# Performance work log

Hardware: AMD Instinct MI355X
Metric: run time of the kernel (lower is better)

Reference implementation:

```python
import jax, jax.numpy as jnp
import numpy as np

FACTOR = 1
EPS = 1e-8
SCALES = (1, 2, 4)


def _pool(x, scale):
    # adaptive_avg_pool1d along time with L % scale == 0 -> uniform bin mean
    if scale == 1:
        return x
    B, L, H, E = x.shape
    return x.reshape(B, L // scale, scale, H, E).mean(axis=2)


def _interp_linear(x, L_out):
    # F.interpolate(mode='linear', align_corners=False) along time axis (axis=1)
    B, Ls, H, E = x.shape
    i = jnp.arange(L_out, dtype=jnp.float32)
    src = jnp.maximum((i + 0.5) * (Ls / L_out) - 0.5, 0.0)
    x0 = jnp.floor(src).astype(jnp.int32)
    x1 = jnp.minimum(x0 + 1, Ls - 1)
    lam = (src - x0.astype(jnp.float32))[None, :, None, None]
    return x[:, x0] * (1.0 - lam) + x[:, x1] * lam


def _corr_agg(q, k, v, w1, b1, w2, b2, w3, b3):
    # q,k,v: [B, Ls, H, E]
    B, Ls, H, E = q.shape
    qf = jnp.fft.rfft(q.transpose(0, 2, 3, 1), axis=-1)   # [B,H,E,Lf]
    kf = jnp.fft.rfft(k.transpose(0, 2, 3, 1), axis=-1)
    corr = jnp.fft.irfft(qf * jnp.conj(kf), n=Ls, axis=-1).astype(jnp.float32)  # [B,H,E,Ls]

    # ---- adaptive-k features ----
    energy = jnp.mean(jnp.sum(corr ** 2, axis=(1, 2)))          # scalar, expanded to B
    var = jnp.var(corr.reshape(B, -1), axis=1, ddof=1)          # unbiased, like torch.var
    cm = corr.reshape(B, H * E, Ls).mean(axis=1)                # [B, Ls]
    pk = jnp.sum((cm[:, 1:-1] > cm[:, :-2]) & (cm[:, 1:-1] > cm[:, 2:]), axis=1).astype(jnp.float32)
    feats = jnp.stack([jnp.broadcast_to(energy, (B,)), var, pk], axis=1)  # [B,3]
    h = jax.nn.relu(feats @ w1.T + b1)
    h = jax.nn.relu(h @ w2.T + b2)
    ratio = jax.nn.sigmoid(h @ w3.T + b3)[:, 0]                 # [B]
    kvals = jnp.clip((ratio * Ls * FACTOR).astype(jnp.int32), 1, Ls)  # [B]

    # ---- adaptive time-delay aggregation ----
    c = corr.transpose(0, 3, 1, 2)                              # [B, Ls, H, E]
    interior = (c[:, 1:-1] > c[:, :-2]) & (c[:, 1:-1] > c[:, 2:])
    pad = jnp.zeros((B, 1, H, E), dtype=bool)
    peaks = jnp.concatenate([pad, interior, pad], axis=1)       # [B,Ls,H,E] local maxima

    neg_inf = jnp.float32(-jnp.inf)
    vals = jnp.where(peaks, c, neg_inf).reshape(B, -1)
    count = peaks.reshape(B, -1).sum(axis=1)
    sorted_desc = -jnp.sort(-vals, axis=1)
    thresh = jnp.take_along_axis(sorted_desc, (kvals - 1)[:, None], axis=1)[:, 0]  # k-th largest peak
    topk_mask = peaks & (c >= thresh[:, None, None, None])
    keep_topk = (count > kvals)[:, None, None, None]
    final = jnp.where(keep_topk, topk_mask, peaks)

    attn = jnp.where(final, c, 0.0)
    w = jax.nn.softmax(attn + EPS, axis=1)                      # softmax over time lags
    return w * v                                                # einsum('lhe,lhe->lhe') == elementwise


def setup_inputs() -> dict:
    key = jax.random.key(0)
    ks = jax.random.split(key, 10)
    B, L, H, E = 16, 1024, 8, 64
    return {
        "queries": jax.random.normal(ks[0], (B, L, H, E), jnp.float32),
        "keys": jax.random.normal(ks[1], (B, L, H, E), jnp.float32),
        "values": jax.random.normal(ks[2], (B, L, H, E), jnp.float32),
        "scale_weights": jax.random.normal(ks[3], (3,), jnp.float32) * 0.1 + 1.0 / 3.0,
        "k_w1": jax.random.normal(ks[4], (32, 3), jnp.float32) * 0.1,
        "k_b1": jax.random.normal(ks[5], (32,), jnp.float32) * 0.1,
        "k_w2": jax.random.normal(ks[6], (16, 32), jnp.float32) * 0.1,
        "k_b2": jax.random.normal(ks[7], (16,), jnp.float32) * 0.1,
        "k_w3": jax.random.normal(ks[8], (1, 16), jnp.float32) * 0.1,
        "k_b3": jax.random.normal(ks[9], (1,), jnp.float32) * 0.1,
    }


def reference(queries, keys, values, scale_weights, k_w1, k_b1, k_w2, k_b2, k_w3, k_b3):
    B, L, H, E = queries.shape
    out = jnp.zeros_like(queries)
    for i, scale in enumerate(SCALES):
        q, k, v = _pool(queries, scale), _pool(keys, scale), _pool(values, scale)
        o = _corr_agg(q, k, v, k_w1, k_b1, k_w2, k_b2, k_w3, k_b3)
        if scale > 1:
            o = _interp_linear(o, L)
        out = out + o * scale_weights[i]
    return out
```

## Files before the change

kernel.cpp:

```cpp
#include <hip/hip_runtime.h>
#include <math.h>

typedef unsigned int u32;
typedef unsigned long long u64;

#define B_ 16
#define L_ 1024
#define H_ 8
#define E_ 64
#define C_ 512
#define NB_SEL 8
#define GCH 8
#define TC 32
#define CAPR 160

__device__ __forceinline__ size_t co(int sidx) {
  return sidx == 0 ? 0u : (sidx == 1 ? 8388608u : 12582912u);
}
__device__ __forceinline__ u32 pk_off(int sidx) {
  return sidx == 0 ? 0u : (sidx == 1 ? 3211264u : 4816896u);
}
__device__ __forceinline__ u32 pk_cap(int sidx) { return 200704u >> sidx; }

__device__ __forceinline__ u32 f2key(float f) {
  u32 u = __float_as_uint(f);
  return (u & 0x80000000u) ? ~u : (u | 0x80000000u);
}
__device__ __forceinline__ float key2f(u32 k) {
  u32 u = (k & 0x80000000u) ? (k ^ 0x80000000u) : ~k;
  return __uint_as_float(u);
}

__global__ void k_init(u32* histA, u32* histB, u32* peak_cnt, u32* done,
                       double* s1, double* s2, float* cm) {
  const int gid = blockIdx.x * 256 + threadIdx.x;
  const int gs = gridDim.x * 256;
  for (int i = gid; i < 3 * 16 * 256; i += gs) { histA[i] = 0; histB[i] = 0; }
  for (int i = gid; i < 3 * 16 * 1024; i += gs) cm[i] = 0.f;
  for (int i = gid; i < 3 * 16 * 16; i += gs) peak_cnt[i] = 0;
  for (int i = gid; i < 144; i += gs) done[i] = 0;
  for (int i = gid; i < 48; i += gs) { s1[i] = 0.0; s2[i] = 0.0; }
}

template<int S>
__device__ __forceinline__ float4 pool_load(const float* gp) {
  float4 v = *(const float4*)gp;
  if constexpr (S >= 2) {
    float4 v2 = *(const float4*)(gp + C_);
    v.x += v2.x; v.y += v2.y; v.z += v2.z; v.w += v2.w;
  }
  if constexpr (S == 4) {
    float4 v3 = *(const float4*)(gp + 2 * C_);
    float4 v4 = *(const float4*)(gp + 3 * C_);
    v.x += v3.x + v4.x; v.y += v3.y + v4.y;
    v.z += v3.z + v4.z; v.w += v3.w + v4.w;
  }
  constexpr float sc = (S == 1) ? 1.f : (S == 2) ? 0.5f : 0.25f;
  if constexpr (S >= 2) { v.x *= sc; v.y *= sc; v.z *= sc; v.w *= sc; }
  return v;
}

template<int S>
__launch_bounds__(256, 3)
__global__ void k_corr(const float* __restrict__ Q, const float* __restrict__ K,
                       float* __restrict__ corr) {
  constexpr int LS = 1024 / S;
  constexpr int LMASK = LS - 1;
  constexpr int NCHUNK = LS / TC;
  __shared__ float qs[TC * 64];
  __shared__ float ks[CAPR * 64];
  const int tid = threadIdx.x;
  const int e = tid & 63;
  const int slot32 = __builtin_amdgcn_readfirstlane((tid >> 6) << 5);
  const int bh = blockIdx.x;
  const int tau0 = blockIdx.y << 7;
  const int b = bh >> 3, h = bh & 7;
  const size_t gbase = (size_t)b * L_ * C_ + (size_t)h * 64;
  const int l16 = tid & 15;
  const int rbase = tid >> 4;
  const int bp0 = 96 - slot32;

  float acc[32];
#pragma unroll
  for (int i = 0; i < 32; ++i) acc[i] = 0.f;

  float4 pq0, pq1, pk0, pk1;
  if constexpr (S == 1) {
    pq0 = *(const float4*)(Q + gbase + (size_t)rbase * C_ + l16 * 4);
    pq1 = *(const float4*)(Q + gbase + (size_t)(rbase + 16) * C_ + l16 * 4);
  }

  int cph = 0;
  for (int chunk = 0; chunk < NCHUNK; ++chunk) {
    const int t0 = chunk * TC;
    __syncthreads();
    if constexpr (S == 1) {
      *(float4*)(qs + rbase * 64 + l16 * 4) = pq0;
      *(float4*)(qs + (rbase + 16) * 64 + l16 * 4) = pq1;
      if (chunk == 0) {
#pragma unroll
        for (int it = 0; it < 10; ++it) {
          int l = rbase + it * 16;
          int tk = (l - tau0 - 127 + 2048) & LMASK;
          *(float4*)(ks + l * 64 + l16 * 4) =
              *(const float4*)(K + gbase + (size_t)tk * C_ + l16 * 4);
        }
      } else {
        int sp = cph + 128; if (sp >= CAPR) sp -= CAPR;
        int p0 = sp + rbase;      if (p0 >= CAPR) p0 -= CAPR;
        int p1 = sp + rbase + 16; if (p1 >= CAPR) p1 -= CAPR;
        *(float4*)(ks + p0 * 64 + l16 * 4) = pk0;
        *(float4*)(ks + p1 * 64 + l16 * 4) = pk1;
      }
      __syncthreads();
      if (chunk + 1 < NCHUNK) {
        int t0n = t0 + TC;
        pq0 = *(const float4*)(Q + gbase + (size_t)(t0n + rbase) * C_ + l16 * 4);
        pq1 = *(const float4*)(Q + gbase + (size_t)(t0n + rbase + 16) * C_ + l16 * 4);
        int l0 = t0n + 128 + rbase;
        int tk0 = (l0 - tau0 - 127 + 2048) & LMASK;
        int tk1 = (l0 + 16 - tau0 - 127 + 2048) & LMASK;
        pk0 = *(const float4*)(K + gbase + (size_t)tk0 * C_ + l16 * 4);
        pk1 = *(const float4*)(K + gbase + (size_t)tk1 * C_ + l16 * 4);
      }
    } else {
#pragma unroll
      for (int it = 0; it < 2; ++it) {
        int row = rbase + it * 16;
        int traw = (t0 + row) * S;
        float4 v = pool_load<S>(Q + gbase + (size_t)traw * C_ + l16 * 4);
        *(float4*)(qs + row * 64 + l16 * 4) = v;
      }
      if (chunk == 0) {
#pragma unroll
        for (int it = 0; it < 10; ++it) {
          int l = rbase + it * 16;
          int tk = (l - tau0 - 127 + 2048) & LMASK;
          float4 v = pool_load<S>(K + gbase + (size_t)tk * S * C_ + l16 * 4);
          *(float4*)(ks + l * 64 + l16 * 4) = v;
        }
      } else {
        int sp = cph + 128; if (sp >= CAPR) sp -= CAPR;
#pragma unroll
        for (int it = 0; it < 2; ++it) {
          int row = rbase + it * 16;
          int l = t0 + 128 + row;
          int tk = (l - tau0 - 127 + 2048) & LMASK;
          int p = sp + row; if (p >= CAPR) p -= CAPR;
          float4 v = pool_load<S>(K + gbase + (size_t)tk * S * C_ + l16 * 4);
          *(float4*)(ks + p * 64 + l16 * 4) = v;
        }
      }
      __syncthreads();
    }
    int bp = bp0 + cph; if (bp >= CAPR) bp -= CAPR;
    float km[63];
    if (bp <= CAPR - 47) {
#pragma unroll
      for (int m = 0; m < 47; ++m) km[m] = ks[(bp + m) * 64 + e];
    } else {
#pragma unroll
      for (int m = 0; m < 47; ++m) {
        int p = bp + m; if (p >= CAPR) p -= CAPR;
        km[m] = ks[p * 64 + e];
      }
    }
#pragma unroll
    for (int jt = 0; jt < 16; ++jt) {
      float qv = qs[jt * 64 + e];
#pragma unroll
      for (int i = 0; i < 32; ++i) acc[i] = fmaf(qv, km[31 + jt - i], acc[i]);
    }
    if (bp <= CAPR - 63) {
#pragma unroll
      for (int m = 47; m < 63; ++m) km[m] = ks[(bp + m) * 64 + e];
    } else {
#pragma unroll
      for (int m = 47; m < 63; ++m) {
        int p = bp + m; if (p >= CAPR) p -= CAPR;
        km[m] = ks[p * 64 + e];
      }
    }
#pragma unroll
    for (int jt = 16; jt < 32; ++jt) {
      float qv = qs[jt * 64 + e];
#pragma unroll
      for (int i = 0; i < 32; ++i) acc[i] = fmaf(qv, km[31 + jt - i], acc[i]);
    }
    cph += 32; if (cph >= CAPR) cph -= CAPR;
  }
  __syncthreads();
  float* wt = ks;
#pragma unroll
  for (int i = 0; i < 32; ++i) wt[(slot32 + i) * 65 + e] = acc[i];
  __syncthreads();
  const int to = tid & 127;
  const size_t cbase = ((size_t)b * C_ + (size_t)h * 64) * LS + tau0 + to;
  for (int cr = tid >> 7; cr < 64; cr += 2)
    corr[cbase + (size_t)cr * LS] = wt[to * 65 + cr];
}

__launch_bounds__(256, 4)
__global__ void k_stats(const float* __restrict__ corrbase, float* __restrict__ cm,
                        double* s1, double* s2, u32* peak_cnt, u32* histA,
                        u32* pkbase) {
  __shared__ __align__(16) float rows[GCH * 1024];
  __shared__ u32 hist_s[256];
  __shared__ double red_d[8];
  __shared__ u32 wv[4], wbase[4];
  const int tid = threadIdx.x;
  const int sidx = blockIdx.z;
  const int b = blockIdx.y;
  const int sb = sidx * 16 + b;
  const int Ls = 1024 >> sidx;
  const int c0 = blockIdx.x * GCH;
  const int lane = tid & 63;
  const int wave = tid >> 6;
  hist_s[tid] = 0;
  {
    const float4* src4 =
        (const float4*)(corrbase + co(sidx) + ((size_t)b * C_ + c0) * Ls);
    float4* dst4 = (float4*)rows;
    const int n4 = GCH * Ls / 4;
    for (int i = tid; i < n4; i += 256) dst4[i] = src4[i];
  }
  __syncthreads();
  const int nt = Ls >> 8;
  float cmacc[4] = {0.f, 0.f, 0.f, 0.f};
  double ls1 = 0.0, ls2 = 0.0;
  u32 mycnt = 0;
  for (int g = 0; g < GCH; ++g) {
    const float* row = rows + g * Ls;
    for (int i = 0; i < nt; ++i) {
      int t = tid + (i << 8);
      float v = row[t];
      cmacc[i] += v;
      ls1 += (double)v;
      ls2 += (double)v * (double)v;
      bool pk = (t >= 1) && (t <= Ls - 2) && (v > row[t - 1]) && (v > row[t + 1]);
      if (pk) {
        ++mycnt;
        atomicAdd(&hist_s[f2key(v) >> 24], 1u);
      }
    }
  }
  u32 wc = mycnt;
  for (int off = 32; off; off >>= 1) wc += __shfl_down(wc, off, 64);
  if (lane == 0) wv[wave] = wc;
  __syncthreads();
  if (tid == 0) {
    u32 t = 0;
    for (int w = 0; w < 4; ++w) { wbase[w] = t; t += wv[w]; }
    u32 base = atomicAdd(&peak_cnt[sb * 16], t);
    for (int w = 0; w < 4; ++w) wbase[w] += base;
  }
  __syncthreads();
  const u32 cap = pk_cap(sidx);
  u32* dst_pk = pkbase + pk_off(sidx) + (u32)b * cap;
  u32 off_w = wbase[wave];
  const u64 below = (1ull << lane) - 1ull;
  for (int g = 0; g < GCH; ++g) {
    const float* row = rows + g * Ls;
    for (int i = 0; i < nt; ++i) {
      int t = tid + (i << 8);
      float v = row[t];
      bool pk = (t >= 1) && (t <= Ls - 2) && (v > row[t - 1]) && (v > row[t + 1]);
      u64 mask = __ballot(pk);
      if (pk) {
        u32 idx = off_w + (u32)__popcll(mask & below);
        if (idx < cap) dst_pk[idx] = f2key(v);
      }
      off_w += (u32)__popcll(mask);
    }
  }
  for (int i = 0; i < nt; ++i) {
    int t = tid + (i << 8);
    unsafeAtomicAdd(&cm[sb * 1024 + t], cmacc[i]);
  }
  for (int off = 32; off; off >>= 1) {
    ls1 += __shfl_down(ls1, off, 64);
    ls2 += __shfl_down(ls2, off, 64);
  }
  if (lane == 0) { red_d[wave] = ls1; red_d[4 + wave] = ls2; }
  __syncthreads();
  if (tid == 0) {
    unsafeAtomicAdd(&s1[sb], red_d[0] + red_d[1] + red_d[2] + red_d[3]);
    unsafeAtomicAdd(&s2[sb], red_d[4] + red_d[5] + red_d[6] + red_d[7]);
  }
  if (hist_s[tid]) atomicAdd(&histA[sb * 256 + tid], hist_s[tid]);
}

__global__ void k_mlp(const float* __restrict__ cm, const double* s1,
                      const double* s2, const u32* peak_cnt, const u32* histA,
                      int* rank_s, u32* prefix_s, u32* active, float* thresh,
                      const float* w1, const float* b1, const float* w2,
                      const float* b2, const float* w3, const float* b3) {
  __shared__ float wls[673];
  __shared__ float cmrow[1024];
  __shared__ int red_i[4];
  __shared__ u32 cum[256];
  const int tid = threadIdx.x;
  const int sb = blockIdx.x;
  const int sidx = sb >> 4;
  const int Ls = 1024 >> sidx;
  for (int i = tid; i < 96; i += 256) wls[i] = w1[i];
  for (int i = tid; i < 32; i += 256) wls[96 + i] = b1[i];
  for (int i = tid; i < 512; i += 256) wls[128 + i] = w2[i];
  if (tid < 16) wls[640 + tid] = b2[tid];
  if (tid < 16) wls[656 + tid] = w3[tid];
  if (tid == 0) wls[672] = b3[0];
  for (int i = tid; i < Ls; i += 256) cmrow[i] = cm[sb * 1024 + i];
  __syncthreads();
  int cnt = 0;
  for (int t = 1 + tid; t <= Ls - 2; t += 256) {
    float v = cmrow[t];
    cnt += (v > cmrow[t - 1]) && (v > cmrow[t + 1]);
  }
  for (int off = 32; off; off >>= 1) cnt += __shfl_down(cnt, off, 64);
  if ((tid & 63) == 0) red_i[tid >> 6] = cnt;
  __syncthreads();
  if (tid == 0) {
    double tot = 0.0;
    for (int j = 0; j < 16; ++j) tot += s2[sidx * 16 + j];
    float f0 = (float)(tot / (16.0 * (double)Ls));
    double N = (double)C_ * (double)Ls;
    float f1 = (float)((s2[sb] - s1[sb] * s1[sb] / N) / (N - 1.0));
    float f2 = (float)(red_i[0] + red_i[1] + red_i[2] + red_i[3]);
    float h1[32];
    for (int j = 0; j < 32; ++j)
      h1[j] = fmaxf(0.f, wls[j * 3] * f0 + wls[j * 3 + 1] * f1 + wls[j * 3 + 2] * f2 + wls[96 + j]);
    float h2[16];
    for (int j = 0; j < 16; ++j) {
      float a = wls[640 + j];
      for (int i = 0; i < 32; ++i) a += wls[128 + j * 32 + i] * h1[i];
      h2[j] = fmaxf(0.f, a);
    }
    float z = wls[672];
    for (int i = 0; i < 16; ++i) z += wls[656 + i] * h2[i];
    float ratio = 1.0f / (1.0f + __expf(-z));
    int kv = (int)(ratio * (float)Ls);
    kv = min(max(kv, 1), Ls);
    int cntb = (int)peak_cnt[sb * 16];
    active[sb] = (u32)(cntb > kv);
    thresh[sb] = -INFINITY;
    rank_s[sb] = kv;
    prefix_s[sb] = 0;
  }
  __syncthreads();
  cum[tid] = histA[sb * 256 + tid];
  __syncthreads();
  for (int off = 1; off < 256; off <<= 1) {
    u32 add = (tid + off < 256) ? cum[tid + off] : 0u;
    __syncthreads();
    cum[tid] += add;
    __syncthreads();
  }
  u32 act_b = active[sb];
  u32 r = act_b ? (u32)rank_s[sb] : 0u;
  u32 cc = cum[tid];
  u32 cnext = (tid == 255) ? 0u : cum[tid + 1];
  __syncthreads();
  if (act_b && r > 0 && cc >= r && cnext < r) {
    prefix_s[sb] = (u32)tid << 24;
    rank_s[sb] = (int)(r - cnext);
  }
}

__global__ void k_sel(const u32* __restrict__ pkbase, const u32* peak_cnt,
                      const u32* active, int* rank_s, u32* prefix_s,
                      u32* hist, u32* done, float* thresh, int level) {
  __shared__ u32 hist_s[256];
  __shared__ u32 cum[256];
  __shared__ u32 islast;
  const int tid = threadIdx.x;
  const int sb = blockIdx.x / NB_SEL;
  const int blk = blockIdx.x % NB_SEL;
  const int sidx = sb >> 4;
  hist_s[tid] = 0;
  if (tid == 0) islast = 0;
  __syncthreads();
  const int act = (int)active[sb];
  const u32 cap = pk_cap(sidx);
  u32 cnt = peak_cnt[sb * 16];
  if (cnt > cap) cnt = cap;
  if (act) {
    const u32 pref = prefix_s[sb];
    const int hi_sh = 32 - 8 * level;
    const int b_sh = 24 - 8 * level;
    const u32 lo = (u32)(((u64)cnt * (u64)blk) / NB_SEL);
    const u32 hi = (u32)(((u64)cnt * (u64)(blk + 1)) / NB_SEL);
    const u32* src = pkbase + pk_off(sidx) + (u32)(sb & 15) * cap;
    for (u32 i = lo + tid; i < hi; i += 256) {
      u32 key = src[i];
      if ((key >> hi_sh) == (pref >> hi_sh))
        atomicAdd(&hist_s[(key >> b_sh) & 255u], 1u);
    }
  }
  __syncthreads();
  if (hist_s[tid]) atomicAdd(&hist[sb * 256 + tid], hist_s[tid]);
  __syncthreads();
  if (tid == 0) {
    __threadfence();
    u32 t = atomicAdd(&done[(level - 1) * 48 + sb], 1u);
    if (t == NB_SEL - 1) islast = 1;
  }
  __syncthreads();
  if (!islast) return;
  __threadfence();
  u32 hv = atomicAdd(&hist[sb * 256 + tid], 0u);
  cum[tid] = hv;
  hist[sb * 256 + tid] = 0;
  __syncthreads();
  for (int off = 1; off < 256; off <<= 1) {
    u32 add = (tid + off < 256) ? cum[tid + off] : 0u;
    __syncthreads();
    cum[tid] += add;
    __syncthreads();
  }
  u32 r = act ? (u32)rank_s[sb] : 0u;
  u32 pref2 = act ? prefix_s[sb] : 0u;
  u32 cc = cum[tid];
  u32 cnext = (tid == 255) ? 0u : cum[tid + 1];
  __syncthreads();
  if (act && r > 0 && cc >= r && cnext < r) {
    u32 np = pref2 | ((u32)tid << (24 - 8 * level));
    prefix_s[sb] = np;
    rank_s[sb] = (int)(r - cnext);
    if (level == 3) thresh[sb] = key2f(np);
  }
}

__global__ void k_softstats(const float* __restrict__ corrbase, const float* thresh,
                            float2* __restrict__ mZ) {
  __shared__ float row[1024];
  __shared__ float red_s[8];
  const int tid = threadIdx.x;
  const int bc = blockIdx.x;
  const int sidx = blockIdx.y;
  const int Ls = 1024 >> sidx;
  const float th = thresh[sidx * 16 + (bc >> 9)];
  const float* src = corrbase + co(sidx) + (size_t)bc * Ls;
  for (int t = tid; t < Ls; t += 256) row[t] = src[t];
  __syncthreads();
  float mx = 0.f;
  for (int t = tid; t < Ls; t += 256) {
    float v = row[t];
    bool pk = (t >= 1) && (t <= Ls - 2) && (v > row[t - 1]) && (v > row[t + 1]) && (v >= th);
    if (pk) mx = fmaxf(mx, v);
  }
  for (int off = 32; off; off >>= 1) mx = fmaxf(mx, __shfl_down(mx, off, 64));
  if ((tid & 63) == 0) red_s[tid >> 6] = mx;
  __syncthreads();
  float m = fmaxf(fmaxf(red_s[0], red_s[1]), fmaxf(red_s[2], red_s[3]));
  float zs = 0.f;
  for (int t = tid; t < Ls; t += 256) {
    float v = row[t];
    bool pk = (t >= 1) && (t <= Ls - 2) && (v > row[t - 1]) && (v > row[t + 1]) && (v >= th);
    float a = pk ? v : 0.f;
    zs += __expf(a - m);
  }
  for (int off = 32; off; off >>= 1) zs += __shfl_down(zs, off, 64);
  if ((tid & 63) == 0) red_s[4 + (tid >> 6)] = zs;
  __syncthreads();
  if (tid == 0) {
    float Z = red_s[4] + red_s[5] + red_s[6] + red_s[7];
    mZ[sidx * 8192 + bc] = make_float2(m, 1.0f / Z);
  }
}

__launch_bounds__(256, 4)
__global__ void k_apply(const float* __restrict__ corr, const float* __restrict__ V,
                        const float2* __restrict__ mZ, const float* thresh,
                        float* __restrict__ o, int Ls, int s) {
  __shared__ float ct[64][131];
  __shared__ float m_s[64], rz_s[64];
  const int tid = threadIdx.x;
  const int b = blockIdx.z;
  const int c0 = blockIdx.y << 6;
  const int t0 = blockIdx.x << 7;
  {
    const int row0 = tid >> 7, jc = tid & 127;
    for (int rr = row0; rr < 64; rr += 2) {
      const float* src = corr + ((size_t)b * C_ + c0 + rr) * Ls;
      for (int j = jc; j < 130; j += 128) {
        int t = t0 - 1 + j;
        t = max(0, min(t, Ls - 1));
        ct[rr][j] = src[t];
      }
    }
  }
  if (tid < 64) {
    float2 v = mZ[b * C_ + c0 + tid];
    m_s[tid] = v.x; rz_s[tid] = v.y;
  }
  __syncthreads();
  const float th = thresh[b];
  const int cl = tid & 63, ts = tid >> 6;
  for (int ii = 0; ii < 32; ++ii) {
    int tl = ts + (ii << 2);
    int tg = t0 + tl;
    float vm = ct[cl][tl], vc = ct[cl][tl + 1], vp = ct[cl][tl + 2];
    bool pk = (tg >= 1) && (tg <= Ls - 2) && (vc > vm) && (vc > vp) && (vc >= th);
    float a = pk ? vc : 0.f;
    float w = __expf(a - m_s[cl]) * rz_s[cl];
    size_t vb = ((size_t)b * L_ + (size_t)tg * s) * C_ + c0 + cl;
    float vv;
    if (s == 2) vv = (V[vb] + V[vb + C_]) * 0.5f;
    else vv = ((V[vb] + V[vb + C_]) + (V[vb + 2 * C_] + V[vb + 3 * C_])) * 0.25f;
    o[((size_t)b * Ls + tg) * C_ + c0 + cl] = w * vv;
  }
}

__launch_bounds__(256, 4)
__global__ void k_apply_final(const float* __restrict__ corr, const float* __restrict__ V,
                              const float2* __restrict__ mZ, const float* thresh,
                              const float* __restrict__ o2, const float* __restrict__ o4,
                              const float* __restrict__ sw, float* __restrict__ out) {
  __shared__ float ct[64][131];
  __shared__ float m_s[64], rz_s[64];
  const int Ls = 1024;
  const int tid = threadIdx.x;
  const int b = blockIdx.z;
  const int c0 = blockIdx.y << 6;
  const int t0 = blockIdx.x << 7;
  {
    const int row0 = tid >> 7, jc = tid & 127;
    for (int rr = row0; rr < 64; rr += 2) {
      const float* src = corr + ((size_t)b * C_ + c0 + rr) * Ls;
      for (int j = jc; j < 130; j += 128) {
        int t = t0 - 1 + j;
        t = max(0, min(t, Ls - 1));
        ct[rr][j] = src[t];
      }
    }
  }
  if (tid < 64) {
    float2 v = mZ[b * C_ + c0 + tid];
    m_s[tid] = v.x; rz_s[tid] = v.y;
  }
  __syncthreads();
  const float th = thresh[b];
  const float sw0 = sw[0], sw1 = sw[1], sw2 = sw[2];
  const int cl = tid & 63, ts = tid >> 6;
  for (int ii = 0; ii < 32; ++ii) {
    int tl = ts + (ii << 2);
    int tg = t0 + tl;
    float vm = ct[cl][tl], vc = ct[cl][tl + 1], vp = ct[cl][tl + 2];
    bool pk = (tg >= 1) && (tg <= Ls - 2) && (vc > vm) && (vc > vp) && (vc >= th);
    float a = pk ? vc : 0.f;
    float w = __expf(a - m_s[cl]) * rz_s[cl];
    float v1 = V[((size_t)b * L_ + tg) * C_ + c0 + cl];
    float r = sw0 * w * v1;
    {
      float srcp = fmaxf((tg + 0.5f) * 0.5f - 0.5f, 0.f);
      int x0 = (int)srcp;
      float lam = srcp - (float)x0;
      int x1 = min(x0 + 1, 511);
      const float* p = o2 + (size_t)b * 512 * C_ + c0 + cl;
      r += sw1 * ((1.f - lam) * p[(size_t)x0 * C_] + lam * p[(size_t)x1 * C_]);
    }
    {
      float srcp = fmaxf((tg + 0.5f) * 0.25f - 0.5f, 0.f);
      int x0 = (int)srcp;
      float lam = srcp - (float)x0;
      int x1 = min(x0 + 1, 255);
      const float* p = o4 + (size_t)b * 256 * C_ + c0 + cl;
      r += sw2 * ((1.f - lam) * p[(size_t)x0 * C_] + lam * p[(size_t)x1 * C_]);
    }
    out[((size_t)b * L_ + tg) * C_ + c0 + cl] = r;
  }
}

extern "C" void kernel_launch(void* const* d_in, const int* in_sizes, int n_in,
                              void* d_out, int out_size, void* d_ws, size_t ws_size,
                              hipStream_t stream) {
  const float* Q  = (const float*)d_in[0];
  const float* Kk = (const float*)d_in[1];
  const float* V  = (const float*)d_in[2];
  const float* sw = (const float*)d_in[3];
  const float* w1 = (const float*)d_in[4];
  const float* b1 = (const float*)d_in[5];
  const float* w2 = (const float*)d_in[6];
  const float* b2 = (const float*)d_in[7];
  const float* w3 = (const float*)d_in[8];
  const float* b3 = (const float*)d_in[9];
  float* out = (float*)d_out;

  char* ws = (char*)d_ws;
  size_t p = 0;
  auto alloc = [&](size_t n) { char* r = ws + p; p = (p + n + 255) & ~(size_t)255; return r; };
  float*  corr = (float*)alloc((size_t)(8388608 + 4194304 + 2097152) * 4);
  char*   oreg = alloc((size_t)25165824);
  float*  o2   = (float*)oreg;
  float*  o4   = (float*)(oreg + 16777216);
  u32*    pk   = (u32*)oreg;
  float*  cm       = (float*)alloc(3 * 16 * 1024 * 4);
  float2* mZ       = (float2*)alloc(3 * 16 * 512 * 8);
  double* s1d      = (double*)alloc(48 * 8);
  double* s2d      = (double*)alloc(48 * 8);
  u32*    histA    = (u32*)alloc(3 * 16 * 256 * 4);
  u32*    histB    = (u32*)alloc(3 * 16 * 256 * 4);
  u32*    peak_cnt = (u32*)alloc(3 * 16 * 16 * 4);
  u32*    done     = (u32*)alloc(144 * 4);
  int*    rank_s   = (int*)alloc(48 * 4);
  u32*    prefix_s = (u32*)alloc(48 * 4);
  u32*    active   = (u32*)alloc(48 * 4);
  float*  thresh   = (float*)alloc(48 * 4);

  k_init<<<dim3(16), dim3(256), 0, stream>>>(histA, histB, peak_cnt, done,
                                             s1d, s2d, cm);
  k_corr<1><<<dim3(128, 8), dim3(256), 0, stream>>>(Q, Kk, corr);
  k_corr<2><<<dim3(128, 4), dim3(256), 0, stream>>>(Q, Kk, corr + 8388608);
  k_corr<4><<<dim3(128, 2), dim3(256), 0, stream>>>(Q, Kk, corr + 12582912);
  k_stats<<<dim3(C_ / GCH, B_, 3), dim3(256), 0, stream>>>(
      corr, cm, s1d, s2d, peak_cnt, histA, pk);
  k_mlp<<<dim3(48), dim3(256), 0, stream>>>(
      cm, s1d, s2d, peak_cnt, histA, rank_s, prefix_s, active, thresh,
      w1, b1, w2, b2, w3, b3);
  for (int level = 1; level <= 3; ++level)
    k_sel<<<dim3(48 * NB_SEL), dim3(256), 0, stream>>>(
        pk, peak_cnt, active, rank_s, prefix_s, histB, done, thresh, level);
  k_softstats<<<dim3(8192, 3), dim3(256), 0, stream>>>(corr, thresh, mZ);
  k_apply<<<dim3(2, 8, 16), dim3(256), 0, stream>>>(
      corr + 12582912, V, mZ + 2 * 8192, thresh + 32, o4, 256, 4);
  k_apply<<<dim3(4, 8, 16), dim3(256), 0, stream>>>(
      corr + 8388608, V, mZ + 1 * 8192, thresh + 16, o2, 512, 2);
  k_apply_final<<<dim3(8, 8, 16), dim3(256), 0, stream>>>(
      corr, V, mZ, thresh, o2, o4, sw, out);
}
```

Measured before the change: 799.5 us.

## Add dedicated scale-1 correlation kernel with async global-to-LDS loads and ring buffer

Replaces the generic templated correlation kernel for the scale-1 level with a specialised kernel. It streams K through a circular LDS ring buffer and double-buffers Q chunks using direct global-to-LDS loads, so the next chunk is prefetched while the current one is accumulated. K windows are held in registers and reused across the 32 time-lag outputs. The aim is to hide memory latency in the largest correlation pass, at the cost of more registers, more LDS use and ring-wraparound branches.

```diff
diff --git a/kernel.cpp b/kernel.cpp
--- a/kernel.cpp
+++ b/kernel.cpp
@@ -13,6 +13,7 @@
 #define GCH 8
 #define TC 32
 #define CAPR 160
+#define CAP1 192
 
 __device__ __forceinline__ size_t co(int sidx) {
   return sidx == 0 ? 0u : (sidx == 1 ? 8388608u : 12582912u);
@@ -29,6 +30,12 @@
 __device__ __forceinline__ float key2f(u32 k) {
   u32 u = (k & 0x80000000u) ? (k ^ 0x80000000u) : ~k;
   return __uint_as_float(u);
+}
+
+using u32g = __attribute__((address_space(1))) const unsigned int;
+using u32l = __attribute__((address_space(3))) unsigned int;
+__device__ __forceinline__ void gload16(const float* g, float* l) {
+  __builtin_amdgcn_global_load_lds((u32g*)g, (u32l*)l, 16, 0, 0);
 }
 
 __global__ void k_init(u32* histA, u32* histB, u32* peak_cnt, u32* done,
@@ -40,6 +47,103 @@
   for (int i = gid; i < 3 * 16 * 16; i += gs) peak_cnt[i] = 0;
   for (int i = gid; i < 144; i += gs) done[i] = 0;
   for (int i = gid; i < 48; i += gs) { s1[i] = 0.0; s2[i] = 0.0; }
+}
+
+__launch_bounds__(256, 2)
+__global__ void k_corr1(const float* __restrict__ Q, const float* __restrict__ K,
+                        float* __restrict__ corr) {
+  constexpr int LS = 1024;
+  constexpr int LMASK = LS - 1;
+  constexpr int NCHUNK = LS / TC;
+  __shared__ float qs[2 * TC * 64];
+  __shared__ float ks[CAP1 * 64];
+  const int tid = threadIdx.x;
+  const int e = tid & 63;
+  const int slot32 = __builtin_amdgcn_readfirstlane((tid >> 6) << 5);
+  const int wb = __builtin_amdgcn_readfirstlane((tid >> 6) << 8);
+  const int bh = blockIdx.x;
+  const int tau0 = blockIdx.y << 7;
+  const int b = bh >> 3, h = bh & 7;
+  const size_t gbase = (size_t)b * L_ * C_ + (size_t)h * 64;
+  const int l16 = tid & 15;
+  const int rbase = tid >> 4;
+  const int bp0 = 96 - slot32;
+
+  float acc[32];
+#pragma unroll
+  for (int i = 0; i < 32; ++i) acc[i] = 0.f;
+
+#pragma unroll
+  for (int it = 0; it < 10; ++it) {
+    int l = it * 16 + rbase;
+    int tk = (l - tau0 - 127 + 2048) & LMASK;
+    gload16(K + gbase + (size_t)tk * C_ + l16 * 4, ks + it * 1024 + wb);
+  }
+  gload16(Q + gbase + (size_t)rbase * C_ + l16 * 4, qs + wb);
+  gload16(Q + gbase + (size_t)(rbase + 16) * C_ + l16 * 4, qs + 1024 + wb);
+  __syncthreads();
+
+  int cph = 0;
+  for (int chunk = 0; chunk < NCHUNK; ++chunk) {
+    if (chunk + 1 < NCHUNK) {
+      const int t0n = (chunk + 1) << 5;
+      float* qn = qs + ((chunk + 1) & 1) * 2048;
+      gload16(Q + gbase + (size_t)(t0n + rbase) * C_ + l16 * 4, qn + wb);
+      gload16(Q + gbase + (size_t)(t0n + rbase + 16) * C_ + l16 * 4, qn + 1024 + wb);
+      const int l0 = (chunk << 5) + 160;
+      int tk0 = (l0 + rbase - tau0 - 127 + 2048) & LMASK;
+      int tk1 = (l0 + rbase + 16 - tau0 - 127 + 2048) & LMASK;
+      int p0 = cph + 160; if (p0 >= CAP1) p0 -= CAP1;
+      int p1 = cph + 176; if (p1 >= CAP1) p1 -= CAP1;
+      gload16(K + gbase + (size_t)tk0 * C_ + l16 * 4, ks + p0 * 64 + wb);
+      gload16(K + gbase + (size_t)tk1 * C_ + l16 * 4, ks + p1 * 64 + wb);
+    }
+    const float* qcur = qs + (chunk & 1) * 2048;
+    int bp = bp0 + cph; if (bp >= CAP1) bp -= CAP1;
+    float km[63];
+    if (bp <= CAP1 - 47) {
+#pragma unroll
+      for (int m = 0; m < 47; ++m) km[m] = ks[(bp + m) * 64 + e];
+    } else {
+#pragma unroll
+      for (int m = 0; m < 47; ++m) {
+        int p = bp + m; if (p >= CAP1) p -= CAP1;
+        km[m] = ks[p * 64 + e];
+      }
+    }
+#pragma unroll
+    for (int jt = 0; jt < 16; ++jt) {
+      float qv = qcur[jt * 64 + e];
+#pragma unroll
+      for (int i = 0; i < 32; ++i) acc[i] = fmaf(qv, km[31 + jt - i], acc[i]);
+    }
+    if (bp <= CAP1 - 63) {
+#pragma unroll
+      for (int m = 47; m < 63; ++m) km[m] = ks[(bp + m) * 64 + e];
+    } else {
+#pragma unroll
+      for (int m = 47; m < 63; ++m) {
+        int p = bp + m; if (p >= CAP1) p -= CAP1;
+        km[m] = ks[p * 64 + e];
+      }
+    }
+#pragma unroll
+    for (int jt = 16; jt < 32; ++jt) {
+      float qv = qcur[jt * 64 + e];
+#pragma unroll
+      for (int i = 0; i < 32; ++i) acc[i] = fmaf(qv, km[31 + jt - i], acc[i]);
+    }
+    __syncthreads();
+    cph += 32; if (cph >= CAP1) cph -= CAP1;
+  }
+  float* wt = ks;
+#pragma unroll
+  for (int i = 0; i < 32; ++i) wt[(slot32 + i) * 65 + e] = acc[i];
+  __syncthreads();
+  const int to = tid & 127;
+  const size_t cbase = ((size_t)b * C_ + (size_t)h * 64) * LS + tau0 + to;
+  for (int cr = tid >> 7; cr < 64; cr += 2)
+    corr[cbase + (size_t)cr * LS] = wt[to * 65 + cr];
 }
 
 template<int S>
@@ -609,7 +713,7 @@
 
   k_init<<<dim3(16), dim3(256), 0, stream>>>(histA, histB, peak_cnt, done,
                                              s1d, s2d, cm);
-  k_corr<1><<<dim3(128, 8), dim3(256), 0, stream>>>(Q, Kk, corr);
+  k_corr1<<<dim3(128, 8), dim3(256), 0, stream>>>(Q, Kk, corr);
   k_corr<2><<<dim3(128, 4), dim3(256), 0, stream>>>(Q, Kk, corr + 8388608);
   k_corr<4><<<dim3(128, 2), dim3(256), 0, stream>>>(Q, Kk, corr + 12582912);
   k_stats<<<dim3(C_ / GCH, B_, 3), dim3(256), 0, stream>>>(
```

Result: no change. 798.1 us (-0.2%).
